# Optimization experiments

Hardware: AMD Instinct MI355X
Metric: run time of the kernel (lower is better)

Reference implementation:

```python
import jax, jax.numpy as jnp
import numpy as np

N = 100000
E = 1600000
D_IN = 128
F = 128


def _glorot(key, shape, scale=1.0):
    fan_in, fan_out = shape
    std = jnp.sqrt(2.0 / (fan_in + fan_out))
    return jax.random.normal(key, shape, dtype=jnp.float32) * std * scale


def setup_inputs() -> dict:
    key = jax.random.key(0)
    ks = jax.random.split(key, 10)
    h = jax.random.normal(ks[0], (N, D_IN), dtype=jnp.float32)
    # ensure every node appears as a row (src) so degree >= 1 (no inf in deg**-0.5)
    src_extra = jax.random.randint(ks[1], (E - N,), 0, N, dtype=jnp.int32)
    edge_src = jnp.concatenate([jnp.arange(N, dtype=jnp.int32), src_extra])
    edge_dst = jax.random.randint(ks[2], (E,), 0, N, dtype=jnp.int32)
    # faithful to original: fake indices sampled in [0, E) (jnp indexing clamps)
    src_fake = jax.random.randint(ks[3], (E,), 0, E, dtype=jnp.int32)
    dst_fake = jax.random.randint(ks[4], (E,), 0, E, dtype=jnp.int32)
    w_gcn0 = _glorot(ks[5], (D_IN, F))
    w_gcn1 = _glorot(ks[6], (F, F))
    # small scale on rate0 head to keep exp(sum over F dims) finite in fp32
    w_rate0 = _glorot(ks[7], (F, F), scale=0.05)
    w_rate1 = _glorot(ks[8], (F, 1))
    w_alpha = _glorot(ks[9], (F, 1))
    return {"h": h, "w_gcn0": w_gcn0, "w_gcn1": w_gcn1, "w_rate0": w_rate0,
            "w_rate1": w_rate1, "w_alpha": w_alpha, "edge_src": edge_src,
            "edge_dst": edge_dst, "src_fake": src_fake, "dst_fake": dst_fake}


def _gcn(h, W, norm, edge_src, edge_dst):
    h = h * norm                     # [N, d] degree pre-norm
    h = h @ W                        # dense projection
    h = jax.ops.segment_sum(h[edge_dst], edge_src, num_segments=N)  # a @ h
    return h * norm                  # degree post-norm


def reference(h, w_gcn0, w_gcn1, w_rate0, w_rate1, w_alpha,
              edge_src, edge_dst, src_fake, dst_fake):
    ones = jnp.ones((E,), dtype=h.dtype)
    deg = jax.ops.segment_sum(ones, edge_src, num_segments=N)  # row sums of a
    norm = (deg ** -0.5)[:, None]

    h = _gcn(h, w_gcn0, norm, edge_src, edge_dst)
    h = _gcn(h, w_gcn1, norm, edge_src, edge_dst)

    rate0 = h @ w_rate0   # [N, F]
    rate1 = h @ w_rate1   # [N, 1]
    alpha = h @ w_alpha   # [N, 1]

    src, dst = edge_src, edge_dst
    rate0_real = jnp.exp((rate0[src] + rate0[dst]).sum(-1))
    rate1_real = jnp.exp((rate1[src] + rate1[dst]).sum(-1))
    alpha_real = jax.nn.sigmoid((alpha[src] * alpha[dst]).sum(-1) / alpha.shape[-1] ** 0.5)

    # faithful to original (including rate0+rate1 mix and /shape (not sqrt) in alpha_fake)
    rate0_fake = jnp.exp((rate0[src_fake] + rate1[dst_fake]).sum(-1))
    rate1_fake = jnp.exp((rate1[src_fake] + rate1[dst_fake]).sum(-1))
    alpha_fake = jax.nn.sigmoid((alpha[src] * alpha[dst_fake]).sum(-1) / alpha.shape[-1])

    return jnp.stack([rate0_real, rate1_real, alpha_real,
                      rate0_fake, rate1_fake, alpha_fake])  # [6, E]
```

## Files before the change

kernel.cpp:

```cpp
#include <hip/hip_runtime.h>
#include <hip/hip_bf16.h>
#include <math.h>

#define NN 100000
#define EE 1600000
#define KB 256
#define RR 391
#define CAP 8192


__global__ __launch_bounds__(256) void k_initcur(int* __restrict__ gcur) {
    gcur[threadIdx.x] = threadIdx.x * CAP;
}


__global__ __launch_bounds__(256) void k_partA(const int* __restrict__ src, const int* __restrict__ dst,
                                               int* __restrict__ gcur, unsigned int* __restrict__ pk, int E) {
    __shared__ int cnt[KB];
    __shared__ int base[KB];
    int t = threadIdx.x;
    int e0 = blockIdx.x * 4096;
    cnt[t] = 0;
    __syncthreads();
    unsigned int pkv[16];
    int bkt[16];
    #pragma unroll
    for (int i = 0; i < 16; ++i) {
        int e = e0 + i * 256 + t;
        if (e < E) {
            int s = src[e];
            int d = dst[e];
            int b = s / RR;
            bkt[i] = b;
            pkv[i] = (unsigned int)d | ((unsigned int)(s - b * RR) << 17);
            atomicAdd(&cnt[b], 1);
        } else {
            bkt[i] = -1;
        }
    }
    __syncthreads();
    base[t] = (cnt[t] > 0) ? atomicAdd(&gcur[t], cnt[t]) : 0;
    __syncthreads();
    cnt[t] = 0;
    __syncthreads();
    #pragma unroll
    for (int i = 0; i < 16; ++i) {
        if (bkt[i] >= 0) {
            int r = atomicAdd(&cnt[bkt[i]], 1);
            int pos = base[bkt[i]] + r;
            if (pos < (bkt[i] + 1) * CAP) pk[pos] = pkv[i];
        }
    }
}


__global__ __launch_bounds__(128) void k_pmat(const float* __restrict__ w_gcn0,
                                              const float* __restrict__ w_gcn1,
                                              const float* __restrict__ w_rate0,
                                              const float* __restrict__ w_rate1,
                                              const float* __restrict__ w_alpha,
                                              float* __restrict__ Pt0, float* __restrict__ Pt1,
                                              float* __restrict__ Pt2) {
    __shared__ float V0[128], V1[128], V2[128];
    __shared__ float Q0[128], Q1[128], Q2[128];
    int t = threadIdx.x;
    float s = 0.f;
    for (int j = 0; j < 128; ++j) s += w_rate0[t * 128 + j];
    V0[t] = s;
    V1[t] = w_rate1[t];
    V2[t] = w_alpha[t];
    __syncthreads();
    {
        float q0 = 0.f, q1 = 0.f, q2 = 0.f;
        for (int k = 0; k < 128; ++k) {
            float w = w_gcn1[t * 128 + k];
            q0 += w * V0[k];
            q1 += w * V1[k];
            q2 += w * V2[k];
        }
        Q0[t] = q0; Q1[t] = q1; Q2[t] = q2;
    }
    __syncthreads();
    {
        float p0 = 0.f, p1 = 0.f, p2 = 0.f;
        for (int m = 0; m < 128; ++m) {
            float w = w_gcn0[t * 128 + m];
            p0 += w * Q0[m];
            p1 += w * Q1[m];
            p2 += w * Q2[m];
        }
        Pt0[t] = p0; Pt1[t] = p1; Pt2[t] = p2;
    }
}


__global__ __launch_bounds__(1024) void k_cnt_proj(const unsigned int* __restrict__ pk,
                                                   const int* __restrict__ gcur,
                                                   const float* __restrict__ h,
                                                   const float* __restrict__ Pt0, const float* __restrict__ Pt1,
                                                   const float* __restrict__ Pt2,
                                                   float* __restrict__ nrm, float4* __restrict__ w4, int n) {
    __shared__ int c[RR];
    __shared__ float s_nrm[RR];
    __shared__ float sP0[128], sP1[128], sP2[128];
    int b = blockIdx.x;
    int t = threadIdx.x;
    int nlo = b * RR;
    int nhi = nlo + RR; if (nhi > n) nhi = n;
    if (nlo >= n) return;
    int nn = nhi - nlo;
    if (t < 128) { sP0[t] = Pt0[t]; sP1[t] = Pt1[t]; sP2[t] = Pt2[t]; }
    for (int i = t; i < RR; i += 1024) c[i] = 0;
    __syncthreads();
    int P0 = b * CAP;
    int m = gcur[b] - P0;
    for (int i = t; i < m; i += 1024) atomicAdd(&c[pk[P0 + i] >> 17], 1);
    __syncthreads();
    for (int i = t; i < nn; i += 1024) {
        float nv = rsqrtf((float)c[i]);
        s_nrm[i] = nv;
        nrm[nlo + i] = nv;
    }
    __syncthreads();
    int hw = t >> 5;
    int l32 = t & 31;
    int c4 = l32 * 4;
    float4 c0 = *(const float4*)(sP0 + c4);
    float4 c1 = *(const float4*)(sP1 + c4);
    float4 c2 = *(const float4*)(sP2 + c4);
    for (int i0 = 0; i0 < nn; i0 += 32) {
        int i = i0 + hw;
        if (i >= nn) break;
        int node = nlo + i;
        float4 hv = *(const float4*)(h + (size_t)node * 128 + c4);
        float p0 = hv.x * c0.x + hv.y * c0.y + hv.z * c0.z + hv.w * c0.w;
        float p1 = hv.x * c1.x + hv.y * c1.y + hv.z * c1.z + hv.w * c1.w;
        float p2 = hv.x * c2.x + hv.y * c2.y + hv.z * c2.z + hv.w * c2.w;
        #pragma unroll
        for (int off = 16; off > 0; off >>= 1) {
            p0 += __shfl_down(p0, off, 32);
            p1 += __shfl_down(p1, off, 32);
            p2 += __shfl_down(p2, off, 32);
        }
        if (l32 == 0) {
            float nv = s_nrm[i];
            w4[node] = make_float4(nv * p0, nv * p1, nv * p2, 0.f);
        }
    }
}


__global__ __launch_bounds__(1024) void k_agg(const unsigned int* __restrict__ pk,
                                              const int* __restrict__ gcur,
                                              const float4* __restrict__ T, const float* __restrict__ nrm,
                                              float4* __restrict__ outv, int n, int mode) {
    __shared__ float s0[RR], s1[RR], s2[RR];
    int b = blockIdx.x;
    int t = threadIdx.x;
    int nlo = b * RR;
    int nhi = nlo + RR; if (nhi > n) nhi = n;
    if (nlo >= n) return;
    for (int i = t; i < RR; i += 1024) { s0[i] = 0.f; s1[i] = 0.f; s2[i] = 0.f; }
    __syncthreads();
    int P0 = b * CAP;
    int m = gcur[b] - P0;
    for (int i = t; i < m; i += 1024) {
        unsigned int w = pk[P0 + i];
        int srel = (int)(w >> 17);
        float4 v = T[w & 0x1FFFFu];
        atomicAdd(&s0[srel], v.x);
        atomicAdd(&s1[srel], v.y);
        atomicAdd(&s2[srel], v.z);
    }
    __syncthreads();
    int nn = nhi - nlo;
    for (int i = t; i < nn; i += 1024) {
        int node = nlo + i;
        float nv = nrm[node];
        float sc = (mode == 1) ? nv * nv : nv;
        outv[node] = make_float4(sc * s0[i], sc * s1[i], sc * s2[i], 0.f);
    }
}


__global__ __launch_bounds__(256) void k_edge_out(const int* __restrict__ esrc, const int* __restrict__ edst,
                                                  const int* __restrict__ sfake, const int* __restrict__ dfake,
                                                  const float4* __restrict__ p4, float* __restrict__ out,
                                                  int E, int n) {
    int e = blockIdx.x * 256 + threadIdx.x;
    if (e >= E) return;
    int s = esrc[e], d = edst[e];
    int sf = sfake[e]; sf = sf < 0 ? 0 : (sf >= n ? n - 1 : sf);
    int df = dfake[e]; df = df < 0 ? 0 : (df >= n ? n - 1 : df);
    float4 ps = p4[s], pd = p4[d], psf = p4[sf], pdf = p4[df];
    out[e]                 = expf(ps.x + pd.x);
    out[(size_t)E + e]     = expf(ps.y + pd.y);
    out[(size_t)2 * E + e] = 1.f / (1.f + expf(-(ps.z * pd.z)));
    out[(size_t)3 * E + e] = expf(psf.x + 128.f * pdf.y);
    out[(size_t)4 * E + e] = expf(psf.y + pdf.y);
    out[(size_t)5 * E + e] = 1.f / (1.f + expf(-(ps.z * pdf.z)));
}


extern "C" void kernel_launch(void* const* d_in, const int* in_sizes, int n_in,
                              void* d_out, int out_size, void* d_ws, size_t ws_size,
                              hipStream_t stream) {
    const float* h       = (const float*)d_in[0];
    const float* w_gcn0  = (const float*)d_in[1];
    const float* w_gcn1  = (const float*)d_in[2];
    const float* w_rate0 = (const float*)d_in[3];
    const float* w_rate1 = (const float*)d_in[4];
    const float* w_alpha = (const float*)d_in[5];
    const int* edge_src  = (const int*)d_in[6];
    const int* edge_dst  = (const int*)d_in[7];
    const int* src_fake  = (const int*)d_in[8];
    const int* dst_fake  = (const int*)d_in[9];
    float* out = (float*)d_out;

    const int N = NN, E = EE;

    char* p = (char*)d_ws;
    auto alloc = [&](size_t bytes) {
        char* r = p;
        p += (bytes + 255) & ~(size_t)255;
        return r;
    };
    unsigned int* pk = (unsigned int*)alloc((size_t)KB * CAP * 4);
    int* gcur   = (int*)alloc(KB * 4);
    float* nrm  = (float*)alloc((size_t)N * 4);
    float4* w4  = (float4*)alloc((size_t)N * 16);
    float4* z4  = (float4*)alloc((size_t)N * 16);
    float4* p4  = (float4*)alloc((size_t)N * 16);
    float* Pt0  = (float*)alloc(512);
    float* Pt1  = (float*)alloc(512);
    float* Pt2  = (float*)alloc(512);

    int ebl4k = (E + 4095) / 4096;
    int ebl = (E + 255) / 256;

    k_initcur<<<1, KB, 0, stream>>>(gcur);
    k_partA<<<ebl4k, 256, 0, stream>>>(edge_src, edge_dst, gcur, pk, E);
    k_pmat<<<1, 128, 0, stream>>>(w_gcn0, w_gcn1, w_rate0, w_rate1, w_alpha, Pt0, Pt1, Pt2);
    k_cnt_proj<<<KB, 1024, 0, stream>>>(pk, gcur, h, Pt0, Pt1, Pt2, nrm, w4, N);
    k_agg<<<KB, 1024, 0, stream>>>(pk, gcur, w4, nrm, z4, N, 1);
    k_agg<<<KB, 1024, 0, stream>>>(pk, gcur, z4, nrm, p4, N, 2);
    k_edge_out<<<ebl, 256, 0, stream>>>(edge_src, edge_dst, src_fake, dst_fake, p4, out, E, N);
}
```

Before: 241.6 us.

## Fuse pipeline into one cooperative megakernel with grid syncs

Replaces the six separate launches with a small prep kernel plus one cooperative kernel of 256 blocks by 1024 threads. Inside it, the h projection (192 blocks) runs at the same time as edge bucketing (64 blocks). Degree counting, the two aggregations and the edge outputs then follow, separated by grid.sync calls. This removes launch gaps and the dependency bubbles between stages. The cost is lower parallelism during partitioning, since 64 blocks now handle what 391 blocks did before, plus grid-barrier overhead and the need for all blocks to be co-resident.

Result: slower. 383.8 us (+58.9%).

```diff
diff --git a/kernel.cpp b/kernel.cpp
--- a/kernel.cpp
+++ b/kernel.cpp
@@ -1,204 +1,205 @@
 #include <hip/hip_runtime.h>
+#include <hip/hip_cooperative_groups.h>
 #include <hip/hip_bf16.h>
 #include <math.h>
+
+namespace cg = cooperative_groups;
 
 #define NN 100000
 #define EE 1600000
 #define KB 256
 #define RR 391
 #define CAP 8192
-
-
-__global__ __launch_bounds__(256) void k_initcur(int* __restrict__ gcur) {
-    gcur[threadIdx.x] = threadIdx.x * CAP;
-}
-
-
-__global__ __launch_bounds__(256) void k_partA(const int* __restrict__ src, const int* __restrict__ dst,
-                                               int* __restrict__ gcur, unsigned int* __restrict__ pk, int E) {
-    __shared__ int cnt[KB];
-    __shared__ int base[KB];
+#define NPROJ 192
+#define NPART 64
+#define EPB 25000
+
+
+__global__ __launch_bounds__(256) void k_pre(const float* __restrict__ w_gcn0,
+                                             const float* __restrict__ w_gcn1,
+                                             const float* __restrict__ w_rate0,
+                                             const float* __restrict__ w_rate1,
+                                             const float* __restrict__ w_alpha,
+                                             float* __restrict__ P, int* __restrict__ gcur) {
     int t = threadIdx.x;
-    int e0 = blockIdx.x * 4096;
-    cnt[t] = 0;
-    __syncthreads();
-    unsigned int pkv[16];
-    int bkt[16];
-    #pragma unroll
-    for (int i = 0; i < 16; ++i) {
-        int e = e0 + i * 256 + t;
-        if (e < E) {
-            int s = src[e];
-            int d = dst[e];
-            int b = s / RR;
-            bkt[i] = b;
-            pkv[i] = (unsigned int)d | ((unsigned int)(s - b * RR) << 17);
-            atomicAdd(&cnt[b], 1);
-        } else {
-            bkt[i] = -1;
-        }
-    }
-    __syncthreads();
-    base[t] = (cnt[t] > 0) ? atomicAdd(&gcur[t], cnt[t]) : 0;
-    __syncthreads();
-    cnt[t] = 0;
-    __syncthreads();
-    #pragma unroll
-    for (int i = 0; i < 16; ++i) {
-        if (bkt[i] >= 0) {
-            int r = atomicAdd(&cnt[bkt[i]], 1);
-            int pos = base[bkt[i]] + r;
-            if (pos < (bkt[i] + 1) * CAP) pk[pos] = pkv[i];
-        }
-    }
-}
-
-
-__global__ __launch_bounds__(128) void k_pmat(const float* __restrict__ w_gcn0,
-                                              const float* __restrict__ w_gcn1,
-                                              const float* __restrict__ w_rate0,
-                                              const float* __restrict__ w_rate1,
-                                              const float* __restrict__ w_alpha,
-                                              float* __restrict__ Pt0, float* __restrict__ Pt1,
-                                              float* __restrict__ Pt2) {
+    if (blockIdx.x == 1) { gcur[t] = t * CAP; return; }
     __shared__ float V0[128], V1[128], V2[128];
     __shared__ float Q0[128], Q1[128], Q2[128];
-    int t = threadIdx.x;
-    float s = 0.f;
-    for (int j = 0; j < 128; ++j) s += w_rate0[t * 128 + j];
-    V0[t] = s;
-    V1[t] = w_rate1[t];
-    V2[t] = w_alpha[t];
+    if (t < 128) {
+        float s = 0.f;
+        for (int j = 0; j < 128; ++j) s += w_rate0[t * 128 + j];
+        V0[t] = s; V1[t] = w_rate1[t]; V2[t] = w_alpha[t];
+    }
     __syncthreads();
-    {
+    if (t < 128) {
         float q0 = 0.f, q1 = 0.f, q2 = 0.f;
         for (int k = 0; k < 128; ++k) {
             float w = w_gcn1[t * 128 + k];
-            q0 += w * V0[k];
-            q1 += w * V1[k];
-            q2 += w * V2[k];
+            q0 += w * V0[k]; q1 += w * V1[k]; q2 += w * V2[k];
         }
         Q0[t] = q0; Q1[t] = q1; Q2[t] = q2;
     }
     __syncthreads();
-    {
+    if (t < 128) {
         float p0 = 0.f, p1 = 0.f, p2 = 0.f;
         for (int m = 0; m < 128; ++m) {
             float w = w_gcn0[t * 128 + m];
-            p0 += w * Q0[m];
-            p1 += w * Q1[m];
-            p2 += w * Q2[m];
-        }
-        Pt0[t] = p0; Pt1[t] = p1; Pt2[t] = p2;
+            p0 += w * Q0[m]; p1 += w * Q1[m]; p2 += w * Q2[m];
+        }
+        P[t] = p0; P[128 + t] = p1; P[256 + t] = p2;
     }
 }
 
 
-__global__ __launch_bounds__(1024) void k_cnt_proj(const unsigned int* __restrict__ pk,
-                                                   const int* __restrict__ gcur,
-                                                   const float* __restrict__ h,
-                                                   const float* __restrict__ Pt0, const float* __restrict__ Pt1,
-                                                   const float* __restrict__ Pt2,
-                                                   float* __restrict__ nrm, float4* __restrict__ w4, int n) {
-    __shared__ int c[RR];
-    __shared__ float s_nrm[RR];
-    __shared__ float sP0[128], sP1[128], sP2[128];
-    int b = blockIdx.x;
-    int t = threadIdx.x;
-    int nlo = b * RR;
-    int nhi = nlo + RR; if (nhi > n) nhi = n;
-    if (nlo >= n) return;
-    int nn = nhi - nlo;
-    if (t < 128) { sP0[t] = Pt0[t]; sP1[t] = Pt1[t]; sP2[t] = Pt2[t]; }
-    for (int i = t; i < RR; i += 1024) c[i] = 0;
-    __syncthreads();
-    int P0 = b * CAP;
-    int m = gcur[b] - P0;
-    for (int i = t; i < m; i += 1024) atomicAdd(&c[pk[P0 + i] >> 17], 1);
-    __syncthreads();
-    for (int i = t; i < nn; i += 1024) {
-        float nv = rsqrtf((float)c[i]);
-        s_nrm[i] = nv;
-        nrm[nlo + i] = nv;
-    }
-    __syncthreads();
-    int hw = t >> 5;
-    int l32 = t & 31;
-    int c4 = l32 * 4;
-    float4 c0 = *(const float4*)(sP0 + c4);
-    float4 c1 = *(const float4*)(sP1 + c4);
-    float4 c2 = *(const float4*)(sP2 + c4);
-    for (int i0 = 0; i0 < nn; i0 += 32) {
-        int i = i0 + hw;
-        if (i >= nn) break;
-        int node = nlo + i;
-        float4 hv = *(const float4*)(h + (size_t)node * 128 + c4);
-        float p0 = hv.x * c0.x + hv.y * c0.y + hv.z * c0.z + hv.w * c0.w;
-        float p1 = hv.x * c1.x + hv.y * c1.y + hv.z * c1.z + hv.w * c1.w;
-        float p2 = hv.x * c2.x + hv.y * c2.y + hv.z * c2.z + hv.w * c2.w;
-        #pragma unroll
-        for (int off = 16; off > 0; off >>= 1) {
-            p0 += __shfl_down(p0, off, 32);
-            p1 += __shfl_down(p1, off, 32);
-            p2 += __shfl_down(p2, off, 32);
-        }
-        if (l32 == 0) {
-            float nv = s_nrm[i];
-            w4[node] = make_float4(nv * p0, nv * p1, nv * p2, 0.f);
-        }
-    }
-}
-
-
-__global__ __launch_bounds__(1024) void k_agg(const unsigned int* __restrict__ pk,
-                                              const int* __restrict__ gcur,
-                                              const float4* __restrict__ T, const float* __restrict__ nrm,
-                                              float4* __restrict__ outv, int n, int mode) {
+__global__ __launch_bounds__(1024) void k_mega(const float* __restrict__ h,
+                                               const int* __restrict__ esrc, const int* __restrict__ edst,
+                                               const int* __restrict__ sfake, const int* __restrict__ dfake,
+                                               const float* __restrict__ P,
+                                               int* __restrict__ gcur, unsigned int* __restrict__ pk,
+                                               float4* __restrict__ u4, float4* __restrict__ w4,
+                                               float4* __restrict__ z4, float4* __restrict__ p4,
+                                               float* __restrict__ out) {
+    cg::grid_group grid = cg::this_grid();
+    const int b = blockIdx.x;
+    const int t = threadIdx.x;
+
+    __shared__ int   hcnt[KB];
+    __shared__ int   hbase[KB];
+    __shared__ int   ci[RR];
+    __shared__ float sn[RR];
     __shared__ float s0[RR], s1[RR], s2[RR];
-    int b = blockIdx.x;
-    int t = threadIdx.x;
-    int nlo = b * RR;
-    int nhi = nlo + RR; if (nhi > n) nhi = n;
-    if (nlo >= n) return;
-    for (int i = t; i < RR; i += 1024) { s0[i] = 0.f; s1[i] = 0.f; s2[i] = 0.f; }
-    __syncthreads();
-    int P0 = b * CAP;
-    int m = gcur[b] - P0;
-    for (int i = t; i < m; i += 1024) {
-        unsigned int w = pk[P0 + i];
-        int srel = (int)(w >> 17);
-        float4 v = T[w & 0x1FFFFu];
-        atomicAdd(&s0[srel], v.x);
-        atomicAdd(&s1[srel], v.y);
-        atomicAdd(&s2[srel], v.z);
-    }
-    __syncthreads();
-    int nn = nhi - nlo;
-    for (int i = t; i < nn; i += 1024) {
-        int node = nlo + i;
-        float nv = nrm[node];
-        float sc = (mode == 1) ? nv * nv : nv;
-        outv[node] = make_float4(sc * s0[i], sc * s1[i], sc * s2[i], 0.f);
-    }
-}
-
-
-__global__ __launch_bounds__(256) void k_edge_out(const int* __restrict__ esrc, const int* __restrict__ edst,
-                                                  const int* __restrict__ sfake, const int* __restrict__ dfake,
-                                                  const float4* __restrict__ p4, float* __restrict__ out,
-                                                  int E, int n) {
-    int e = blockIdx.x * 256 + threadIdx.x;
-    if (e >= E) return;
-    int s = esrc[e], d = edst[e];
-    int sf = sfake[e]; sf = sf < 0 ? 0 : (sf >= n ? n - 1 : sf);
-    int df = dfake[e]; df = df < 0 ? 0 : (df >= n ? n - 1 : df);
-    float4 ps = p4[s], pd = p4[d], psf = p4[sf], pdf = p4[df];
-    out[e]                 = expf(ps.x + pd.x);
-    out[(size_t)E + e]     = expf(ps.y + pd.y);
-    out[(size_t)2 * E + e] = 1.f / (1.f + expf(-(ps.z * pd.z)));
-    out[(size_t)3 * E + e] = expf(psf.x + 128.f * pdf.y);
-    out[(size_t)4 * E + e] = expf(psf.y + pdf.y);
-    out[(size_t)5 * E + e] = 1.f / (1.f + expf(-(ps.z * pdf.z)));
+    __shared__ float sP[384];
+
+    if (b < NPROJ) {
+        if (t < 384) sP[t] = P[t];
+        __syncthreads();
+        int l32 = t & 31, hw = t >> 5, c4 = l32 * 4;
+        float4 c0 = *(const float4*)(sP + c4);
+        float4 c1 = *(const float4*)(sP + 128 + c4);
+        float4 c2 = *(const float4*)(sP + 256 + c4);
+        for (int node = b * 32 + hw; node < NN; node += NPROJ * 32) {
+            float4 hv = *(const float4*)(h + (size_t)node * 128 + c4);
+            float p0 = hv.x * c0.x + hv.y * c0.y + hv.z * c0.z + hv.w * c0.w;
+            float p1 = hv.x * c1.x + hv.y * c1.y + hv.z * c1.z + hv.w * c1.w;
+            float p2 = hv.x * c2.x + hv.y * c2.y + hv.z * c2.z + hv.w * c2.w;
+            #pragma unroll
+            for (int off = 16; off > 0; off >>= 1) {
+                p0 += __shfl_down(p0, off, 32);
+                p1 += __shfl_down(p1, off, 32);
+                p2 += __shfl_down(p2, off, 32);
+            }
+            if (l32 == 0) u4[node] = make_float4(p0, p1, p2, 0.f);
+        }
+    } else {
+        int pb = b - NPROJ;
+        int elo = pb * EPB;
+        int ehi = elo + EPB; if (ehi > EE) ehi = EE;
+        for (int be = elo; be < ehi; be += 8192) {
+            if (t < KB) hcnt[t] = 0;
+            __syncthreads();
+            unsigned int pkv[8];
+            int bkt[8];
+            #pragma unroll
+            for (int i = 0; i < 8; ++i) {
+                int e = be + i * 1024 + t;
+                if (e < ehi) {
+                    int s = esrc[e];
+                    int d = edst[e];
+                    int bk = s / RR;
+                    bkt[i] = bk;
+                    pkv[i] = (unsigned int)d | ((unsigned int)(s - bk * RR) << 17);
+                    atomicAdd(&hcnt[bk], 1);
+                } else bkt[i] = -1;
+            }
+            __syncthreads();
+            if (t < KB) hbase[t] = (hcnt[t] > 0) ? atomicAdd(&gcur[t], hcnt[t]) : 0;
+            __syncthreads();
+            if (t < KB) hcnt[t] = 0;
+            __syncthreads();
+            #pragma unroll
+            for (int i = 0; i < 8; ++i) {
+                if (bkt[i] >= 0) {
+                    int r = atomicAdd(&hcnt[bkt[i]], 1);
+                    int pos = hbase[bkt[i]] + r;
+                    if (pos < (bkt[i] + 1) * CAP) pk[pos] = pkv[i];
+                }
+            }
+            __syncthreads();
+        }
+    }
+    grid.sync();
+
+    const int nlo = b * RR;
+    int nhi = nlo + RR; if (nhi > NN) nhi = NN;
+    const int nn = nhi - nlo;
+    const int P0 = b * CAP;
+    int m = gcur[b] - P0; if (m > CAP) m = CAP;
+    {
+        for (int i = t; i < RR; i += 1024) ci[i] = 0;
+        __syncthreads();
+        for (int i = t; i < m; i += 1024) atomicAdd(&ci[pk[P0 + i] >> 17], 1);
+        __syncthreads();
+        for (int i = t; i < nn; i += 1024) {
+            float nv = rsqrtf((float)ci[i]);
+            sn[i] = nv;
+            float4 uu = u4[nlo + i];
+            w4[nlo + i] = make_float4(nv * uu.x, nv * uu.y, nv * uu.z, 0.f);
+        }
+    }
+    grid.sync();
+
+    {
+        for (int i = t; i < RR; i += 1024) { s0[i] = 0.f; s1[i] = 0.f; s2[i] = 0.f; }
+        __syncthreads();
+        for (int i = t; i < m; i += 1024) {
+            unsigned int w = pk[P0 + i];
+            int srel = (int)(w >> 17);
+            float4 v = w4[w & 0x1FFFFu];
+            atomicAdd(&s0[srel], v.x);
+            atomicAdd(&s1[srel], v.y);
+            atomicAdd(&s2[srel], v.z);
+        }
+        __syncthreads();
+        for (int i = t; i < nn; i += 1024) {
+            float nv = sn[i];
+            float sc = nv * nv;
+            z4[nlo + i] = make_float4(sc * s0[i], sc * s1[i], sc * s2[i], 0.f);
+        }
+    }
+    grid.sync();
+
+    {
+        __syncthreads();
+        for (int i = t; i < RR; i += 1024) { s0[i] = 0.f; s1[i] = 0.f; s2[i] = 0.f; }
+        __syncthreads();
+        for (int i = t; i < m; i += 1024) {
+            unsigned int w = pk[P0 + i];
+            int srel = (int)(w >> 17);
+            float4 v = z4[w & 0x1FFFFu];
+            atomicAdd(&s0[srel], v.x);
+            atomicAdd(&s1[srel], v.y);
+            atomicAdd(&s2[srel], v.z);
+        }
+        __syncthreads();
+        for (int i = t; i < nn; i += 1024) {
+            float nv = sn[i];
+            p4[nlo + i] = make_float4(nv * s0[i], nv * s1[i], nv * s2[i], 0.f);
+        }
+    }
+    grid.sync();
+
+    for (int e = b * 1024 + t; e < EE; e += KB * 1024) {
+        int s = esrc[e], d = edst[e];
+        int sf = sfake[e]; sf = sf < 0 ? 0 : (sf >= NN ? NN - 1 : sf);
+        int df = dfake[e]; df = df < 0 ? 0 : (df >= NN ? NN - 1 : df);
+        float4 ps = p4[s], pd = p4[d], psf = p4[sf], pdf = p4[df];
+        out[e]                  = expf(ps.x + pd.x);
+        out[(size_t)EE + e]     = expf(ps.y + pd.y);
+        out[(size_t)2 * EE + e] = 1.f / (1.f + expf(-(ps.z * pd.z)));
+        out[(size_t)3 * EE + e] = expf(psf.x + 128.f * pdf.y);
+        out[(size_t)4 * EE + e] = expf(psf.y + pdf.y);
+        out[(size_t)5 * EE + e] = 1.f / (1.f + expf(-(ps.z * pdf.z)));
+    }
 }
 
 
@@ -217,8 +218,6 @@
     const int* dst_fake  = (const int*)d_in[9];
     float* out = (float*)d_out;
 
-    const int N = NN, E = EE;
-
     char* p = (char*)d_ws;
     auto alloc = [&](size_t bytes) {
         char* r = p;
@@ -227,22 +226,16 @@
     };
     unsigned int* pk = (unsigned int*)alloc((size_t)KB * CAP * 4);
     int* gcur   = (int*)alloc(KB * 4);
-    float* nrm  = (float*)alloc((size_t)N * 4);
-    float4* w4  = (float4*)alloc((size_t)N * 16);
-    float4* z4  = (float4*)alloc((size_t)N * 16);
-    float4* p4  = (float4*)alloc((size_t)N * 16);
-    float* Pt0  = (float*)alloc(512);
-    float* Pt1  = (float*)alloc(512);
-    float* Pt2  = (float*)alloc(512);
-
-    int ebl4k = (E + 4095) / 4096;
-    int ebl = (E + 255) / 256;
-
-    k_initcur<<<1, KB, 0, stream>>>(gcur);
-    k_partA<<<ebl4k, 256, 0, stream>>>(edge_src, edge_dst, gcur, pk, E);
-    k_pmat<<<1, 128, 0, stream>>>(w_gcn0, w_gcn1, w_rate0, w_rate1, w_alpha, Pt0, Pt1, Pt2);
-    k_cnt_proj<<<KB, 1024, 0, stream>>>(pk, gcur, h, Pt0, Pt1, Pt2, nrm, w4, N);
-    k_agg<<<KB, 1024, 0, stream>>>(pk, gcur, w4, nrm, z4, N, 1);
-    k_agg<<<KB, 1024, 0, stream>>>(pk, gcur, z4, nrm, p4, N, 2);
-    k_edge_out<<<ebl, 256, 0, stream>>>(edge_src, edge_dst, src_fake, dst_fake, p4, out, E, N);
+    float* P    = (float*)alloc(384 * 4);
+    float4* u4  = (float4*)alloc((size_t)NN * 16);
+    float4* w4  = (float4*)alloc((size_t)NN * 16);
+    float4* z4  = (float4*)alloc((size_t)NN * 16);
+    float4* p4  = (float4*)alloc((size_t)NN * 16);
+
+    k_pre<<<2, 256, 0, stream>>>(w_gcn0, w_gcn1, w_rate0, w_rate1, w_alpha, P, gcur);
+
+    void* args[] = { (void*)&h, (void*)&edge_src, (void*)&edge_dst, (void*)&src_fake, (void*)&dst_fake,
+                     (void*)&P, (void*)&gcur, (void*)&pk, (void*)&u4, (void*)&w4, (void*)&z4, (void*)&p4,
+                     (void*)&out };
+    hipLaunchCooperativeKernel((void*)k_mega, dim3(KB), dim3(1024), args, 0, stream);
 }
```
